# Kernel optimization log

Hardware: AMD Instinct MI355X
Metric: run time of the kernel (lower is better)

Reference implementation:

```python
import jax, jax.numpy as jnp
import numpy as np

B, N, C, H = 2, 2048, 1024, 16
D = C // H
SCALE = D ** -0.5


def setup_inputs() -> dict:
    key = jax.random.key(0)
    ks = jax.random.split(key, 4)
    s = 0.02
    return {
        "x": jax.random.normal(ks[0], (B, N, C), dtype=jnp.float32),
        "f": jax.random.normal(ks[1], (B, N, C), dtype=jnp.float32),
        "W_qkv": jax.random.normal(ks[2], (C, 3 * C), dtype=jnp.float32) * s,
        "W_proj": jax.random.normal(ks[3], (C, C), dtype=jnp.float32) * s,
        "b_proj": jnp.zeros((C,), dtype=jnp.float32),
    }


def reference(x, f, W_qkv, W_proj, b_proj):
    b, n, c = x.shape
    h, d = H, c // H
    # qkv projection -> (B,N,3,H,D) -> q,k,v each (B,H,N,D)
    qkv = (x @ W_qkv).reshape(b, n, 3, h, d)
    q = jnp.transpose(qkv[:, :, 0], (0, 2, 1, 3))
    k = jnp.transpose(qkv[:, :, 1], (0, 2, 1, 3))
    v = jnp.transpose(qkv[:, :, 2], (0, 2, 1, 3))
    # full NxN scores, faithful to the original manual MHA
    attn = jax.nn.softmax(jnp.einsum("bhqd,bhkd->bhqk", q, k) * SCALE, axis=-1)
    av = jnp.einsum("bhqk,bhkd->bhqd", attn, v)  # (B,H,N,D)
    # pre-residual output branch
    attn2gcn = jnp.transpose(av, (0, 2, 1, 3)).reshape(b, n, c)
    # residual fuse with f (reshaped per-head in torch; equivalent to flat add)
    fused = attn2gcn + f
    out = fused @ W_proj + b_proj
    return (out, attn2gcn)
```

## Files before the change

kernel.cpp:

```cpp
#include <hip/hip_runtime.h>
#include <hip/hip_bf16.h>

#define OUT1_OFF 4194304
#define QSCALE 0.1803368801111204f

typedef __attribute__((ext_vector_type(8))) short bf16x8;
typedef __attribute__((ext_vector_type(4))) float f32x4;

__device__ __forceinline__ unsigned short f2bf(float x) {
    unsigned u = __float_as_uint(x);
    u += 0x7FFFu + ((u >> 16) & 1u);
    return (unsigned short)(u >> 16);
}

__device__ __forceinline__ void gl2lds16(const unsigned short* g, unsigned short* l) {
    __builtin_amdgcn_global_load_lds(
        (const __attribute__((address_space(1))) unsigned int*)g,
        (__attribute__((address_space(3))) unsigned int*)l, 16, 0, 0);
}

__global__ __launch_bounds__(256) void prep(const float* __restrict__ x,
                                            const float* __restrict__ Wqkv,
                                            const float* __restrict__ Wproj,
                                            unsigned short* __restrict__ xb,
                                            unsigned short* __restrict__ wqkvT,
                                            unsigned short* __restrict__ wprojT) {
    __shared__ float T[64][65];
    const int bid = blockIdx.x, tid = threadIdx.x;
    if (bid < 4096) {
        int i = bid * 256 + tid;
        float4 v = reinterpret_cast<const float4*>(x)[i];
        ushort4 o = make_ushort4(f2bf(v.x), f2bf(v.y), f2bf(v.z), f2bf(v.w));
        reinterpret_cast<ushort4*>(xb)[i] = o;
        return;
    }
    const float* in; unsigned short* out; int Nd, bx, by;
    if (bid < 4864) { int t = bid - 4096; in = Wqkv;  out = wqkvT;  Nd = 3072; bx = t % 48; by = t / 48; }
    else            { int t = bid - 4864; in = Wproj; out = wprojT; Nd = 1024; bx = t % 16; by = t / 16; }
    const int Kd = 1024;
    const int r0 = by * 64, c0 = bx * 64;
    const int tr = tid >> 3, tc = (tid & 7) * 8;
#pragma unroll
    for (int rr = 0; rr < 64; rr += 32) {
        const float4* p = reinterpret_cast<const float4*>(&in[(r0 + tr + rr) * Nd + c0 + tc]);
        float4 v0 = p[0], v1 = p[1];
        T[tr + rr][tc + 0] = v0.x; T[tr + rr][tc + 1] = v0.y;
        T[tr + rr][tc + 2] = v0.z; T[tr + rr][tc + 3] = v0.w;
        T[tr + rr][tc + 4] = v1.x; T[tr + rr][tc + 5] = v1.y;
        T[tr + rr][tc + 6] = v1.z; T[tr + rr][tc + 7] = v1.w;
    }
    __syncthreads();
#pragma unroll
    for (int rr = 0; rr < 64; rr += 32) {
        int orow = tr + rr;
        ushort4 o0 = make_ushort4(f2bf(T[tc + 0][orow]), f2bf(T[tc + 1][orow]),
                                  f2bf(T[tc + 2][orow]), f2bf(T[tc + 3][orow]));
        ushort4 o1 = make_ushort4(f2bf(T[tc + 4][orow]), f2bf(T[tc + 5][orow]),
                                  f2bf(T[tc + 6][orow]), f2bf(T[tc + 7][orow]));
        unsigned short* dst = &out[(c0 + orow) * Kd + r0 + tc];
        *reinterpret_cast<ushort4*>(dst) = o0;
        *reinterpret_cast<ushort4*>(dst + 4) = o1;
    }
}

__global__ __launch_bounds__(256) void gemm_qkv(const unsigned short* __restrict__ A,
                                                const unsigned short* __restrict__ Bt,
                                                unsigned short* __restrict__ qb,
                                                unsigned short* __restrict__ kb,
                                                unsigned short* __restrict__ vtb) {
    __shared__ __align__(16) unsigned short Sh[18432];
    unsigned short* As = Sh;
    unsigned short* Bs = Sh + 8192;
    const int tid = threadIdx.x;
    const int w = tid >> 6, lane = tid & 63, quad = lane >> 4, l15 = lane & 15;
    const int m0 = blockIdx.y * 128, n0 = blockIdx.x * 128;
    const int wm = (w & 1) * 64, wn = (w >> 1) * 64;
    const int nbase = n0 + wn;
    const int t = nbase >> 10;
    const bool qk = (t < 2);
    const int sw = (l15 & 7) << 3;
    f32x4 acc[4][4] = {};
    for (int k0 = 0; k0 < 1024; k0 += 64) {
        __syncthreads();
#pragma unroll
        for (int tt = 0; tt < 4; ++tt) {
            int c = tt * 256 + tid;
            int row = c >> 3, jg = ((c & 7) ^ (row & 7)) * 8;
            gl2lds16(&A[(m0 + row) * 1024 + k0 + jg], &As[c * 8]);
            gl2lds16(&Bt[(n0 + row) * 1024 + k0 + jg], &Bs[c * 8]);
        }
        __syncthreads();
#pragma unroll
        for (int kk = 0; kk < 2; ++kk) {
            bf16x8 af[4], bfr[4];
#pragma unroll
            for (int i = 0; i < 4; ++i)
                af[i] = *reinterpret_cast<const bf16x8*>(
                    &As[(wm + i * 16 + l15) * 64 + ((((kk * 4 + quad) << 3) ^ sw))]);
#pragma unroll
            for (int j = 0; j < 4; ++j)
                bfr[j] = *reinterpret_cast<const bf16x8*>(
                    &Bs[(wn + j * 16 + l15) * 64 + ((((kk * 4 + quad) << 3) ^ sw))]);
            if (qk) {
#pragma unroll
                for (int i = 0; i < 4; ++i)
#pragma unroll
                    for (int j = 0; j < 4; ++j)
                        acc[i][j] = __builtin_amdgcn_mfma_f32_16x16x32_bf16(bfr[j], af[i], acc[i][j], 0, 0, 0);
            } else {
#pragma unroll
                for (int i = 0; i < 4; ++i)
#pragma unroll
                    for (int j = 0; j < 4; ++j)
                        acc[i][j] = __builtin_amdgcn_mfma_f32_16x16x32_bf16(af[i], bfr[j], acc[i][j], 0, 0, 0);
            }
        }
    }
    __syncthreads();
    unsigned short* scr = Sh + w * 4608;
    const int mb = m0 + wm;
    const int b = mb >> 11;
    const int h = (nbase & 1023) >> 6;
    const float sc = (t == 0) ? QSCALE : 1.f;
    if (qk) {
#pragma unroll
        for (int i = 0; i < 4; ++i) {
            int row = i * 16 + l15;
#pragma unroll
            for (int j = 0; j < 4; ++j) {
                unsigned short h0 = f2bf(acc[i][j][0] * sc), h1 = f2bf(acc[i][j][1] * sc);
                unsigned short h2 = f2bf(acc[i][j][2] * sc), h3 = f2bf(acc[i][j][3] * sc);
                uint2 pk = make_uint2((unsigned)h0 | ((unsigned)h1 << 16),
                                      (unsigned)h2 | ((unsigned)h3 << 16));
                *reinterpret_cast<uint2*>(&scr[row * 72 + j * 16 + quad * 4]) = pk;
            }
        }
        asm volatile("s_waitcnt lgkmcnt(0)" ::: "memory");
        unsigned short* dst = (t == 0 ? qb : kb) + (((b * 16 + h) * 2048) + (mb & 2047)) * 64;
#pragma unroll
        for (int p = 0; p < 8; ++p) {
            int idx = p * 64 + lane;
            *reinterpret_cast<uint4*>(&dst[idx * 8]) =
                *reinterpret_cast<const uint4*>(&scr[(idx >> 3) * 72 + (idx & 7) * 8]);
        }
    } else {
        const int kblk = (mb & 2047) >> 6;
#pragma unroll
        for (int i = 0; i < 4; ++i) {
            int slot0 = ((i & 2) << 4) | (quad << 3) | ((i & 1) << 2);
#pragma unroll
            for (int j = 0; j < 4; ++j) {
                unsigned short h0 = f2bf(acc[i][j][0]), h1 = f2bf(acc[i][j][1]);
                unsigned short h2 = f2bf(acc[i][j][2]), h3 = f2bf(acc[i][j][3]);
                uint2 pk = make_uint2((unsigned)h0 | ((unsigned)h1 << 16),
                                      (unsigned)h2 | ((unsigned)h3 << 16));
                *reinterpret_cast<uint2*>(&scr[(j * 16 + l15) * 72 + slot0]) = pk;
            }
        }
        asm volatile("s_waitcnt lgkmcnt(0)" ::: "memory");
        unsigned short* vtile = vtb + (((b * 16 + h) * 32) + kblk) * 4096;
#pragma unroll
        for (int p = 0; p < 8; ++p) {
            int idx = p * 64 + lane;
            *reinterpret_cast<uint4*>(&vtile[idx * 8]) =
                *reinterpret_cast<const uint4*>(&scr[(idx >> 3) * 72 + (idx & 7) * 8]);
        }
    }
}

__global__ __launch_bounds__(512) void attn_kernel(const unsigned short* __restrict__ qb,
                                                   const unsigned short* __restrict__ kb,
                                                   const unsigned short* __restrict__ vtb,
                                                   const float* __restrict__ f,
                                                   float* __restrict__ attn2_out,
                                                   unsigned short* __restrict__ fusedb) {
    __shared__ __align__(16) unsigned short Ksw[2][4096];
    __shared__ __align__(16) unsigned short Vsw[2][4096];
    const int tid = threadIdx.x;
    const int w = tid >> 6, lane = tid & 63, quad = lane >> 4, l15 = lane & 15;
    const int bh = blockIdx.x;
    const int q0 = blockIdx.y * 128 + w * 16;
    const unsigned short* qr = &qb[(bh * 2048 + q0 + l15) * 64 + quad * 8];
    bf16x8 ql0 = *reinterpret_cast<const bf16x8*>(qr);
    bf16x8 ql1 = *reinterpret_cast<const bf16x8*>(qr + 32);
    const unsigned short* kt0 = kb + bh * 131072;
    const unsigned short* vt0 = vtb + bh * 131072;
    const int c = tid;
    const int gu = (((c & ~7) | ((c & 7) ^ ((c >> 3) & 7))) << 3);
    const int sw = (l15 & 7) << 3;
    f32x4 O[4] = {};
    f32x4 asum = {};
    bf16x8 ones;
#pragma unroll
    for (int j = 0; j < 8; ++j) ones[j] = (short)0x3F80;

#define STAGE(IT, BUF) do { int _toff = (IT) * 4096;                    \
        gl2lds16(kt0 + _toff + gu, &Ksw[BUF][c * 8]);                   \
        gl2lds16(vt0 + _toff + gu, &Vsw[BUF][c * 8]); } while (0)

    auto body = [&](int buf) {
        f32x4 T[4];
#pragma unroll
        for (int s = 0; s < 4; ++s) {
            const unsigned short* kr = &Ksw[buf][(s * 16 + l15) * 64];
            bf16x8 k0 = *reinterpret_cast<const bf16x8*>(&kr[(quad << 3) ^ sw]);
            bf16x8 k1 = *reinterpret_cast<const bf16x8*>(&kr[((quad + 4) << 3) ^ sw]);
            f32x4 z = {};
            z = __builtin_amdgcn_mfma_f32_16x16x32_bf16(k0, ql0, z, 0, 0, 0);
            z = __builtin_amdgcn_mfma_f32_16x16x32_bf16(k1, ql1, z, 0, 0, 0);
            T[s] = z;
        }
        float p[4][4];
#pragma unroll
        for (int s = 0; s < 4; ++s)
#pragma unroll
            for (int r = 0; r < 4; ++r) p[s][r] = __builtin_amdgcn_exp2f(T[s][r]);
        uint4 u0, u1;
        u0.x = __builtin_amdgcn_perm(__float_as_uint(p[0][1]), __float_as_uint(p[0][0]), 0x07060302u);
        u0.y = __builtin_amdgcn_perm(__float_as_uint(p[0][3]), __float_as_uint(p[0][2]), 0x07060302u);
        u0.z = __builtin_amdgcn_perm(__float_as_uint(p[1][1]), __float_as_uint(p[1][0]), 0x07060302u);
        u0.w = __builtin_amdgcn_perm(__float_as_uint(p[1][3]), __float_as_uint(p[1][2]), 0x07060302u);
        u1.x = __builtin_amdgcn_perm(__float_as_uint(p[2][1]), __float_as_uint(p[2][0]), 0x07060302u);
        u1.y = __builtin_amdgcn_perm(__float_as_uint(p[2][3]), __float_as_uint(p[2][2]), 0x07060302u);
        u1.z = __builtin_amdgcn_perm(__float_as_uint(p[3][1]), __float_as_uint(p[3][0]), 0x07060302u);
        u1.w = __builtin_amdgcn_perm(__float_as_uint(p[3][3]), __float_as_uint(p[3][2]), 0x07060302u);
        bf16x8 pa0 = __builtin_bit_cast(bf16x8, u0);
        bf16x8 pa1 = __builtin_bit_cast(bf16x8, u1);
        asum = __builtin_amdgcn_mfma_f32_16x16x32_bf16(pa0, ones, asum, 0, 0, 0);
        asum = __builtin_amdgcn_mfma_f32_16x16x32_bf16(pa1, ones, asum, 0, 0, 0);
#pragma unroll
        for (int c4 = 0; c4 < 4; ++c4) {
            const unsigned short* vr = &Vsw[buf][(c4 * 16 + l15) * 64];
            bf16x8 v0 = *reinterpret_cast<const bf16x8*>(&vr[(quad << 3) ^ sw]);
            bf16x8 v1 = *reinterpret_cast<const bf16x8*>(&vr[((quad + 4) << 3) ^ sw]);
            O[c4] = __builtin_amdgcn_mfma_f32_16x16x32_bf16(pa0, v0, O[c4], 0, 0, 0);
            O[c4] = __builtin_amdgcn_mfma_f32_16x16x32_bf16(pa1, v1, O[c4], 0, 0, 0);
        }
    };

    STAGE(0, 0);
    for (int it = 0; it < 32; it += 2) {
        __syncthreads();
        STAGE(it + 1, 1);
        body(0);
        __syncthreads();
        if (it + 2 < 32) STAGE(it + 2, 0);
        body(1);
    }
#undef STAGE

    const int b = bh >> 4, h = bh & 15;
#pragma unroll
    for (int r = 0; r < 4; ++r) {
        float inv = 1.f / asum[r];
        int tok = q0 + quad * 4 + r;
        int base = (b * 2048 + tok) * 1024 + h * 64;
#pragma unroll
        for (int c4 = 0; c4 < 4; ++c4) {
            int col = c4 * 16 + l15;
            float o = O[c4][r] * inv;
            attn2_out[base + col] = o;
            fusedb[base + col] = f2bf(o + f[base + col]);
        }
    }
}

__global__ __launch_bounds__(256) void gemm_proj(const unsigned short* __restrict__ A,
                                                 const unsigned short* __restrict__ Bt,
                                                 const float* __restrict__ bias,
                                                 float* __restrict__ out) {
    __shared__ __align__(16) unsigned short As[8192];
    __shared__ __align__(16) unsigned short Bs[4096];
    const int tid = threadIdx.x;
    const int w = tid >> 6, lane = tid & 63, quad = lane >> 4, l15 = lane & 15;
    const int m0 = blockIdx.y * 128, n0 = blockIdx.x * 64;
    const int wm = (w & 1) * 64, wn = (w >> 1) * 32;
    const int sw = (l15 & 7) << 3;
    f32x4 acc[4][2] = {};
    for (int k0 = 0; k0 < 1024; k0 += 64) {
        __syncthreads();
#pragma unroll
        for (int t = 0; t < 4; ++t) {
            int c = t * 256 + tid;
            int row = c >> 3, jg = ((c & 7) ^ (row & 7)) * 8;
            gl2lds16(&A[(m0 + row) * 1024 + k0 + jg], &As[c * 8]);
            if (t < 2) gl2lds16(&Bt[(n0 + row) * 1024 + k0 + jg], &Bs[c * 8]);
        }
        __syncthreads();
#pragma unroll
        for (int kk = 0; kk < 2; ++kk) {
            bf16x8 af[4], bfr[2];
#pragma unroll
            for (int i = 0; i < 4; ++i)
                af[i] = *reinterpret_cast<const bf16x8*>(
                    &As[(wm + i * 16 + l15) * 64 + ((((kk * 4 + quad) << 3) ^ sw))]);
#pragma unroll
            for (int j = 0; j < 2; ++j)
                bfr[j] = *reinterpret_cast<const bf16x8*>(
                    &Bs[(wn + j * 16 + l15) * 64 + ((((kk * 4 + quad) << 3) ^ sw))]);
#pragma unroll
            for (int i = 0; i < 4; ++i)
#pragma unroll
                for (int j = 0; j < 2; ++j)
                    acc[i][j] = __builtin_amdgcn_mfma_f32_16x16x32_bf16(af[i], bfr[j], acc[i][j], 0, 0, 0);
        }
    }
#pragma unroll
    for (int j = 0; j < 2; ++j) {
        int n = n0 + wn + j * 16 + l15;
        float bv = bias[n];
#pragma unroll
        for (int i = 0; i < 4; ++i)
#pragma unroll
            for (int r = 0; r < 4; ++r) {
                int m = m0 + wm + i * 16 + quad * 4 + r;
                out[m * 1024 + n] = acc[i][j][r] + bv;
            }
    }
}

extern "C" void kernel_launch(void* const* d_in, const int* in_sizes, int n_in,
                              void* d_out, int out_size, void* d_ws, size_t ws_size,
                              hipStream_t stream) {
    const float* x      = (const float*)d_in[0];
    const float* f      = (const float*)d_in[1];
    const float* W_qkv  = (const float*)d_in[2];
    const float* W_proj = (const float*)d_in[3];
    const float* b_proj = (const float*)d_in[4];
    float* out   = (float*)d_out;
    float* attn2 = out + OUT1_OFF;

    char* ws = (char*)d_ws;
    unsigned short* xb     = (unsigned short*)(ws);
    unsigned short* wqkvT  = (unsigned short*)(ws + 8388608);
    unsigned short* wprojT = (unsigned short*)(ws + 14680064);
    unsigned short* qb     = (unsigned short*)(ws + 16777216);
    unsigned short* kb     = (unsigned short*)(ws + 25165824);
    unsigned short* vtb    = (unsigned short*)(ws + 33554432);
    unsigned short* fusedb = (unsigned short*)(ws + 41943040);

    prep<<<5120, 256, 0, stream>>>(x, W_qkv, W_proj, xb, wqkvT, wprojT);
    gemm_qkv<<<dim3(24, 32), 256, 0, stream>>>(xb, wqkvT, qb, kb, vtb);
    attn_kernel<<<dim3(32, 16), 512, 0, stream>>>(qb, kb, vtb, f, attn2, fusedb);
    gemm_proj<<<dim3(16, 32), 256, 0, stream>>>(fusedb, wprojT, b_proj, out);
}
```

Before: 185.8 us.

## Process two query tiles per wave in attention to reuse K/V LDS reads

```diff
diff --git a/kernel.cpp b/kernel.cpp
--- a/kernel.cpp
+++ b/kernel.cpp
@@ -168,7 +168,7 @@
     }
 }
 
-__global__ __launch_bounds__(512) void attn_kernel(const unsigned short* __restrict__ qb,
+__global__ __launch_bounds__(256) void attn_kernel(const unsigned short* __restrict__ qb,
                                                    const unsigned short* __restrict__ kb,
                                                    const unsigned short* __restrict__ vtb,
                                                    const float* __restrict__ f,
@@ -179,63 +179,91 @@
     const int tid = threadIdx.x;
     const int w = tid >> 6, lane = tid & 63, quad = lane >> 4, l15 = lane & 15;
     const int bh = blockIdx.x;
-    const int q0 = blockIdx.y * 128 + w * 16;
+    const int q0 = blockIdx.y * 128 + w * 32;
     const unsigned short* qr = &qb[(bh * 2048 + q0 + l15) * 64 + quad * 8];
     bf16x8 ql0 = *reinterpret_cast<const bf16x8*>(qr);
     bf16x8 ql1 = *reinterpret_cast<const bf16x8*>(qr + 32);
+    bf16x8 ql2 = *reinterpret_cast<const bf16x8*>(qr + 1024);
+    bf16x8 ql3 = *reinterpret_cast<const bf16x8*>(qr + 1056);
     const unsigned short* kt0 = kb + bh * 131072;
     const unsigned short* vt0 = vtb + bh * 131072;
-    const int c = tid;
-    const int gu = (((c & ~7) | ((c & 7) ^ ((c >> 3) & 7))) << 3);
+    const int c0i = tid, c1i = tid + 256;
+    const int gu0 = (((c0i & ~7) | ((c0i & 7) ^ ((c0i >> 3) & 7))) << 3);
+    const int gu1 = (((c1i & ~7) | ((c1i & 7) ^ ((c1i >> 3) & 7))) << 3);
     const int sw = (l15 & 7) << 3;
-    f32x4 O[4] = {};
-    f32x4 asum = {};
+    f32x4 O0[4] = {}, O1[4] = {};
+    f32x4 asum0 = {}, asum1 = {};
     bf16x8 ones;
 #pragma unroll
     for (int j = 0; j < 8; ++j) ones[j] = (short)0x3F80;
 
 #define STAGE(IT, BUF) do { int _toff = (IT) * 4096;                    \
-        gl2lds16(kt0 + _toff + gu, &Ksw[BUF][c * 8]);                   \
-        gl2lds16(vt0 + _toff + gu, &Vsw[BUF][c * 8]); } while (0)
+        gl2lds16(kt0 + _toff + gu0, &Ksw[BUF][c0i * 8]);                \
+        gl2lds16(vt0 + _toff + gu0, &Vsw[BUF][c0i * 8]);                \
+        gl2lds16(kt0 + _toff + gu1, &Ksw[BUF][c1i * 8]);                \
+        gl2lds16(vt0 + _toff + gu1, &Vsw[BUF][c1i * 8]); } while (0)
 
     auto body = [&](int buf) {
-        f32x4 T[4];
+        f32x4 Ta[4], Tb[4];
+        __builtin_amdgcn_s_setprio(1);
 #pragma unroll
         for (int s = 0; s < 4; ++s) {
             const unsigned short* kr = &Ksw[buf][(s * 16 + l15) * 64];
             bf16x8 k0 = *reinterpret_cast<const bf16x8*>(&kr[(quad << 3) ^ sw]);
             bf16x8 k1 = *reinterpret_cast<const bf16x8*>(&kr[((quad + 4) << 3) ^ sw]);
-            f32x4 z = {};
-            z = __builtin_amdgcn_mfma_f32_16x16x32_bf16(k0, ql0, z, 0, 0, 0);
-            z = __builtin_amdgcn_mfma_f32_16x16x32_bf16(k1, ql1, z, 0, 0, 0);
-            T[s] = z;
-        }
-        float p[4][4];
+            f32x4 za = {}, zb = {};
+            za = __builtin_amdgcn_mfma_f32_16x16x32_bf16(k0, ql0, za, 0, 0, 0);
+            za = __builtin_amdgcn_mfma_f32_16x16x32_bf16(k1, ql1, za, 0, 0, 0);
+            zb = __builtin_amdgcn_mfma_f32_16x16x32_bf16(k0, ql2, zb, 0, 0, 0);
+            zb = __builtin_amdgcn_mfma_f32_16x16x32_bf16(k1, ql3, zb, 0, 0, 0);
+            Ta[s] = za; Tb[s] = zb;
+        }
+        __builtin_amdgcn_s_setprio(0);
+        float pa_[4][4], pb_[4][4];
 #pragma unroll
         for (int s = 0; s < 4; ++s)
 #pragma unroll
-            for (int r = 0; r < 4; ++r) p[s][r] = __builtin_amdgcn_exp2f(T[s][r]);
-        uint4 u0, u1;
-        u0.x = __builtin_amdgcn_perm(__float_as_uint(p[0][1]), __float_as_uint(p[0][0]), 0x07060302u);
-        u0.y = __builtin_amdgcn_perm(__float_as_uint(p[0][3]), __float_as_uint(p[0][2]), 0x07060302u);
-        u0.z = __builtin_amdgcn_perm(__float_as_uint(p[1][1]), __float_as_uint(p[1][0]), 0x07060302u);
-        u0.w = __builtin_amdgcn_perm(__float_as_uint(p[1][3]), __float_as_uint(p[1][2]), 0x07060302u);
-        u1.x = __builtin_amdgcn_perm(__float_as_uint(p[2][1]), __float_as_uint(p[2][0]), 0x07060302u);
-        u1.y = __builtin_amdgcn_perm(__float_as_uint(p[2][3]), __float_as_uint(p[2][2]), 0x07060302u);
-        u1.z = __builtin_amdgcn_perm(__float_as_uint(p[3][1]), __float_as_uint(p[3][0]), 0x07060302u);
-        u1.w = __builtin_amdgcn_perm(__float_as_uint(p[3][3]), __float_as_uint(p[3][2]), 0x07060302u);
-        bf16x8 pa0 = __builtin_bit_cast(bf16x8, u0);
-        bf16x8 pa1 = __builtin_bit_cast(bf16x8, u1);
-        asum = __builtin_amdgcn_mfma_f32_16x16x32_bf16(pa0, ones, asum, 0, 0, 0);
-        asum = __builtin_amdgcn_mfma_f32_16x16x32_bf16(pa1, ones, asum, 0, 0, 0);
+            for (int r = 0; r < 4; ++r) {
+                pa_[s][r] = __builtin_amdgcn_exp2f(Ta[s][r]);
+                pb_[s][r] = __builtin_amdgcn_exp2f(Tb[s][r]);
+            }
+        uint4 u0, u1, v0u, v1u;
+        u0.x = __builtin_amdgcn_perm(__float_as_uint(pa_[0][1]), __float_as_uint(pa_[0][0]), 0x07060302u);
+        u0.y = __builtin_amdgcn_perm(__float_as_uint(pa_[0][3]), __float_as_uint(pa_[0][2]), 0x07060302u);
+        u0.z = __builtin_amdgcn_perm(__float_as_uint(pa_[1][1]), __float_as_uint(pa_[1][0]), 0x07060302u);
+        u0.w = __builtin_amdgcn_perm(__float_as_uint(pa_[1][3]), __float_as_uint(pa_[1][2]), 0x07060302u);
+        u1.x = __builtin_amdgcn_perm(__float_as_uint(pa_[2][1]), __float_as_uint(pa_[2][0]), 0x07060302u);
+        u1.y = __builtin_amdgcn_perm(__float_as_uint(pa_[2][3]), __float_as_uint(pa_[2][2]), 0x07060302u);
+        u1.z = __builtin_amdgcn_perm(__float_as_uint(pa_[3][1]), __float_as_uint(pa_[3][0]), 0x07060302u);
+        u1.w = __builtin_amdgcn_perm(__float_as_uint(pa_[3][3]), __float_as_uint(pa_[3][2]), 0x07060302u);
+        v0u.x = __builtin_amdgcn_perm(__float_as_uint(pb_[0][1]), __float_as_uint(pb_[0][0]), 0x07060302u);
+        v0u.y = __builtin_amdgcn_perm(__float_as_uint(pb_[0][3]), __float_as_uint(pb_[0][2]), 0x07060302u);
+        v0u.z = __builtin_amdgcn_perm(__float_as_uint(pb_[1][1]), __float_as_uint(pb_[1][0]), 0x07060302u);
+        v0u.w = __builtin_amdgcn_perm(__float_as_uint(pb_[1][3]), __float_as_uint(pb_[1][2]), 0x07060302u);
+        v1u.x = __builtin_amdgcn_perm(__float_as_uint(pb_[2][1]), __float_as_uint(pb_[2][0]), 0x07060302u);
+        v1u.y = __builtin_amdgcn_perm(__float_as_uint(pb_[2][3]), __float_as_uint(pb_[2][2]), 0x07060302u);
+        v1u.z = __builtin_amdgcn_perm(__float_as_uint(pb_[3][1]), __float_as_uint(pb_[3][0]), 0x07060302u);
+        v1u.w = __builtin_amdgcn_perm(__float_as_uint(pb_[3][3]), __float_as_uint(pb_[3][2]), 0x07060302u);
+        bf16x8 paa0 = __builtin_bit_cast(bf16x8, u0);
+        bf16x8 paa1 = __builtin_bit_cast(bf16x8, u1);
+        bf16x8 pba0 = __builtin_bit_cast(bf16x8, v0u);
+        bf16x8 pba1 = __builtin_bit_cast(bf16x8, v1u);
+        asum0 = __builtin_amdgcn_mfma_f32_16x16x32_bf16(paa0, ones, asum0, 0, 0, 0);
+        asum0 = __builtin_amdgcn_mfma_f32_16x16x32_bf16(paa1, ones, asum0, 0, 0, 0);
+        asum1 = __builtin_amdgcn_mfma_f32_16x16x32_bf16(pba0, ones, asum1, 0, 0, 0);
+        asum1 = __builtin_amdgcn_mfma_f32_16x16x32_bf16(pba1, ones, asum1, 0, 0, 0);
+        __builtin_amdgcn_s_setprio(1);
 #pragma unroll
         for (int c4 = 0; c4 < 4; ++c4) {
             const unsigned short* vr = &Vsw[buf][(c4 * 16 + l15) * 64];
             bf16x8 v0 = *reinterpret_cast<const bf16x8*>(&vr[(quad << 3) ^ sw]);
             bf16x8 v1 = *reinterpret_cast<const bf16x8*>(&vr[((quad + 4) << 3) ^ sw]);
-            O[c4] = __builtin_amdgcn_mfma_f32_16x16x32_bf16(pa0, v0, O[c4], 0, 0, 0);
-            O[c4] = __builtin_amdgcn_mfma_f32_16x16x32_bf16(pa1, v1, O[c4], 0, 0, 0);
-        }
+            O0[c4] = __builtin_amdgcn_mfma_f32_16x16x32_bf16(paa0, v0, O0[c4], 0, 0, 0);
+            O0[c4] = __builtin_amdgcn_mfma_f32_16x16x32_bf16(paa1, v1, O0[c4], 0, 0, 0);
+            O1[c4] = __builtin_amdgcn_mfma_f32_16x16x32_bf16(pba0, v0, O1[c4], 0, 0, 0);
+            O1[c4] = __builtin_amdgcn_mfma_f32_16x16x32_bf16(pba1, v1, O1[c4], 0, 0, 0);
+        }
+        __builtin_amdgcn_s_setprio(0);
     };
 
     STAGE(0, 0);
@@ -252,15 +280,20 @@
     const int b = bh >> 4, h = bh & 15;
 #pragma unroll
     for (int r = 0; r < 4; ++r) {
-        float inv = 1.f / asum[r];
-        int tok = q0 + quad * 4 + r;
-        int base = (b * 2048 + tok) * 1024 + h * 64;
+        float inv0 = 1.f / asum0[r];
+        float inv1 = 1.f / asum1[r];
+        int tok0 = q0 + quad * 4 + r;
+        int base0 = (b * 2048 + tok0) * 1024 + h * 64;
+        int base1 = base0 + 16 * 1024;
 #pragma unroll
         for (int c4 = 0; c4 < 4; ++c4) {
             int col = c4 * 16 + l15;
-            float o = O[c4][r] * inv;
-            attn2_out[base + col] = o;
-            fusedb[base + col] = f2bf(o + f[base + col]);
+            float o0 = O0[c4][r] * inv0;
+            attn2_out[base0 + col] = o0;
+            fusedb[base0 + col] = f2bf(o0 + f[base0 + col]);
+            float o1 = O1[c4][r] * inv1;
+            attn2_out[base1 + col] = o1;
+            fusedb[base1 + col] = f2bf(o1 + f[base1 + col]);
         }
     }
 }
@@ -341,6 +374,6 @@
 
     prep<<<5120, 256, 0, stream>>>(x, W_qkv, W_proj, xb, wqkvT, wprojT);
     gemm_qkv<<<dim3(24, 32), 256, 0, stream>>>(xb, wqkvT, qb, kb, vtb);
-    attn_kernel<<<dim3(32, 16), 512, 0, stream>>>(qb, kb, vtb, f, attn2, fusedb);
+    attn_kernel<<<dim3(32, 16), 256, 0, stream>>>(qb, kb, vtb, f, attn2, fusedb);
     gemm_proj<<<dim3(16, 32), 256, 0, stream>>>(fusedb, wprojT, b_proj, out);
 }
```

Measured after the change: 191.9 us. 1.03x slower.
